# Performance work log

Measured on AMD Instinct MI355X. Metric: run time of the kernel, lower is better.

Reference implementation:

```python
import jax, jax.numpy as jnp
import numpy as np

ITEM_NUM = 50000
EMBED = 256          # d4 = 64, d2 = 128
HIDDEN = 128
BETA = 0.5
BATCH = 4096
HIST = 50
K_NEAR = 10


def setup_inputs() -> dict:
    key = jax.random.key(0)
    ks = jax.random.split(key, 12)
    d4, d2 = EMBED // 4, EMBED // 2
    return {
        "history": jax.random.randint(ks[0], (BATCH, HIST), 0, ITEM_NUM),
        "target": jax.random.randint(ks[1], (BATCH,), 0, ITEM_NUM),
        "near_pois": jax.random.randint(ks[2], (ITEM_NUM, K_NEAR), 0, ITEM_NUM),
        "target_region": jax.random.randint(ks[3], (BATCH,), 0, 1000),
        "E_in": jax.random.normal(ks[4], (ITEM_NUM, d4), jnp.float32) * 0.01,
        "E_out": jax.random.normal(ks[5], (ITEM_NUM, d4), jnp.float32) * 0.01,
        "E_hist": jax.random.normal(ks[6], (ITEM_NUM, d2), jnp.float32) * 0.01,
        "E_targ": jax.random.normal(ks[7], (ITEM_NUM, d2), jnp.float32) * 0.01,
        "W1": jax.random.normal(ks[8], (HIDDEN, EMBED), jnp.float32) * 0.02,
        "b1": jnp.zeros((HIDDEN,), jnp.float32),
        "W2": jax.random.normal(ks[9], (1, HIDDEN), jnp.float32) * 0.02,
    }


def _self_attn(q_src, kv):
    # q = row 0 of q_src; key is a RESHAPE (not transpose) of kv, faithful to torch code.
    N, K, d = kv.shape
    q = q_src[:, 0:1, :]                      # [N,1,d]
    k = kv.reshape(N, d, K)                   # [N,d,K] (reshape, matching torch)
    scores = jnp.einsum('nod,ndk->nok', q, k) / jnp.sqrt(jnp.float32(d))
    w = jax.nn.softmax(scores, axis=-1)       # [N,1,K]
    return jnp.einsum('nok,nkd->nod', w, kv)[:, 0, :]  # [N,d]


def reference(history, target, near_pois, target_region,
              E_in, E_out, E_hist, E_targ, W1, b1, W2):
    ingoing = E_in[near_pois]                 # [N,K,d4]
    outgoing = E_out[near_pois]               # [N,K,d4]
    region_out = _self_attn(ingoing, outgoing)   # [N,d4]
    region_in = _self_attn(outgoing, ingoing)    # [N,d4]

    hist_region = jnp.concatenate([region_in[history], region_out[history]], -1)  # [B,H,d2]
    targ_region = jnp.concatenate([region_out[target], region_in[target]], -1)    # [B,d2]

    hist = jnp.concatenate([E_hist[history], hist_region], -1)      # [B,H,E]
    targ = jnp.concatenate([E_targ[target], targ_region], -1)       # [B,E]

    x = hist * targ[:, None, :]                                     # [B,H,E]
    h1 = jax.nn.relu(x @ W1.T + b1)                                 # [B,H,hidden] (dropout = eval/identity)
    scores = (h1 @ W2.T)[..., 0]                                    # [B,H]

    mask = (history != target[:, None])
    expA = jnp.exp(scores) * mask                                   # [B,H]
    denom = jnp.sum(expA, axis=-1) ** BETA                          # [B], power-normalized (non-softmax)
    w = expA / denom[:, None]                                       # [B,H]

    pred = jnp.einsum('bhe,bh,be->b', hist, w, targ)                # weighted bmm reduction
    return jax.nn.sigmoid(pred)
```

## Files before the change

### kernel.cpp

```cpp
#include <hip/hip_runtime.h>
#include <hip/hip_bf16.h>
#include <math.h>

#define EMBED 256
#define HIDDEN 128
#define NBATCH 4096
#define HISTN 50
#define KNEAR 10
#define D4 64
#define ITEMN 50000
#define XSB 272
#define RBLK (ITEMN / 4)

#define SH 64.0f
#define SW 32.0f
#define INV_SXSW (1.0f / 32768.0f)
#define INV_SX (1.0f / 1024.0f)

typedef __attribute__((ext_vector_type(4))) float floatx4;
typedef __attribute__((ext_vector_type(2))) float floatx2;
typedef __attribute__((ext_vector_type(2))) __fp16 half2v;

__device__ inline unsigned pkh2(float a, float b) {
    union { half2v h; unsigned u; } cv;
    cv.h = __builtin_amdgcn_cvt_pkrtz(a, b);
    return cv.u;
}
__device__ inline float h2f(unsigned short u) {
    union { unsigned short u; __fp16 h; } cv; cv.u = u;
    return (float)cv.h;
}
__device__ inline unsigned pk_fp8x4(float a, float b, float c, float d) {
    int v = __builtin_amdgcn_cvt_pk_fp8_f32(a, b, 0, false);
    v = __builtin_amdgcn_cvt_pk_fp8_f32(c, d, v, true);
    return (unsigned)v;
}
__device__ inline void up_fp8x4(unsigned u, float* f) {
    floatx2 lo = __builtin_amdgcn_cvt_pk_f32_fp8((int)u, false);
    floatx2 hi = __builtin_amdgcn_cvt_pk_f32_fp8((int)u, true);
    f[0] = lo.x; f[1] = lo.y; f[2] = hi.x; f[3] = hi.y;
}

template<int CTRL>
__device__ __forceinline__ float dppf(float x) {
    return __uint_as_float((unsigned)__builtin_amdgcn_update_dpp(
        0, (int)__float_as_uint(x), CTRL, 0xF, 0xF, true));
}
#define DPP_XOR1 0xB1
#define DPP_XOR2 0x4E
#define DPP_HMIR 0x141
#define DPP_MIR  0x140

__global__ __launch_bounds__(256) void prep_eio(
    const float* __restrict__ E_in, const float* __restrict__ E_out,
    unsigned short* __restrict__ EioT)
{
    int tid = blockIdx.x * 256 + threadIdx.x;
    int row = tid >> 4, c = tid & 15;
    const float* src = (c < 8) ? &E_in[(size_t)row * 64 + (c & 7) * 8]
                               : &E_out[(size_t)row * 64 + (c & 7) * 8];
    float4 a = ((const float4*)src)[0];
    float4 b = ((const float4*)src)[1];
    uint4 o;
    o.x = pkh2(a.x, a.y); o.y = pkh2(a.z, a.w);
    o.z = pkh2(b.x, b.y); o.w = pkh2(b.z, b.w);
    *(uint4*)&EioT[(size_t)row * 128 + c * 8] = o;
}

__global__ __launch_bounds__(256) void regions3(
    const int* __restrict__ np,
    const unsigned short* __restrict__ EioT,
    const float* __restrict__ E_hist, const float* __restrict__ W1,
    unsigned char* __restrict__ histT, unsigned char* __restrict__ W1s)
{
    __shared__ unsigned short tiles[4][2][KNEAR * D4];

    if (blockIdx.x < RBLK) {
        const int wv = threadIdx.x >> 6;
        const int lane = threadIdx.x & 63;
        const int n = blockIdx.x * 4 + wv;
        const int g16 = lane >> 4, c16 = lane & 15;
        const int half = c16 >> 3, col = (c16 & 7) * 8;

#pragma unroll
        for (int j = 0; j < 3; ++j) {
            int r = j * 4 + g16;
            if (r < KNEAR) {
                int item = np[n * KNEAR + r];
                uint4 v = *(const uint4*)&EioT[(size_t)item * 128 + c16 * 8];
                *(uint4*)&tiles[wv][half][r * 64 + col] = v;
            }
        }
        __asm__ volatile("s_waitcnt lgkmcnt(0)" ::: "memory");

        const int kk = c16;
        const int par = lane & 1, cp = lane >> 1;

#pragma unroll
        for (int pass = 0; pass < 2; ++pass) {
            const unsigned short* qrow = tiles[wv][pass];
            const unsigned short* kvt = tiles[wv][1 - pass];

            float qf[16];
            {
                uint4 qa = *(const uint4*)&qrow[g16 * 16];
                uint4 qb = *(const uint4*)&qrow[g16 * 16 + 8];
                unsigned wd[8] = {qa.x, qa.y, qa.z, qa.w, qb.x, qb.y, qb.z, qb.w};
#pragma unroll
                for (int m = 0; m < 8; ++m) {
                    qf[2 * m]     = h2f((unsigned short)(wd[m] & 0xffff));
                    qf[2 * m + 1] = h2f((unsigned short)(wd[m] >> 16));
                }
            }

            const unsigned short* kvp = &kvt[g16 * 160 + kk];
            float p = 0.f;
#pragma unroll
            for (int i = 0; i < 16; ++i)
                p = fmaf(h2f(kvp[10 * i]), qf[i], p);
            p += __shfl_xor(p, 16);
            p += __shfl_xor(p, 32);
            float sc = p * 0.125f;

            float mv = (kk < 10) ? sc : -1e30f;
            mv = fmaxf(mv, dppf<DPP_XOR1>(mv));
            mv = fmaxf(mv, dppf<DPP_XOR2>(mv));
            mv = fmaxf(mv, dppf<DPP_HMIR>(mv));
            mv = fmaxf(mv, dppf<DPP_MIR>(mv));
            float e = (kk < 10) ? __expf(sc - mv) : 0.f;
            float s = e;
            s += dppf<DPP_XOR1>(s);
            s += dppf<DPP_XOR2>(s);
            s += dppf<DPP_HMIR>(s);
            s += dppf<DPP_MIR>(s);
            float w = e / s;

            float oc0 = 0.f, oc1 = 0.f;
#pragma unroll
            for (int q = 0; q < 5; ++q) {
                float we = __uint_as_float(__builtin_amdgcn_readlane(__float_as_uint(w), 2 * q));
                float wo = __uint_as_float(__builtin_amdgcn_readlane(__float_as_uint(w), 2 * q + 1));
                float ws = par ? wo : we;
                unsigned v = *(const unsigned*)&kvt[(2 * q + par) * 64 + cp * 2];
                oc0 = fmaf(h2f((unsigned short)(v & 0xffff)), ws, oc0);
                oc1 = fmaf(h2f((unsigned short)(v >> 16)), ws, oc1);
            }
            oc0 += dppf<DPP_XOR1>(oc0);
            oc1 += dppf<DPP_XOR1>(oc1);
            if (!par) {
                unsigned char* dst = histT + (size_t)n * 256
                                     + (pass ? 128 : 192) + cp * 2;
                int v2 = __builtin_amdgcn_cvt_pk_fp8_f32(oc0 * SH, oc1 * SH, 0, false);
                *(unsigned short*)dst = (unsigned short)(v2 & 0xffff);
            }
        }
        return;
    }

    long t = (long)(blockIdx.x - RBLK) * 256 + threadIdx.x;
    if (t < (long)ITEMN * 16) {
        int row = (int)(t >> 4);
        int c8 = ((int)t & 15) * 8;
        const float4* s = (const float4*)&E_hist[(size_t)row * 128 + c8];
        float4 a = s[0], b = s[1];
        uint2 o;
        o.x = pk_fp8x4(a.x * SH, a.y * SH, a.z * SH, a.w * SH);
        o.y = pk_fp8x4(b.x * SH, b.y * SH, b.z * SH, b.w * SH);
        *(uint2*)&histT[(size_t)row * 256 + c8] = o;
        return;
    }
    t -= (long)ITEMN * 16;
    if (t < 4096) {
        int l = (int)t & 63;
        int f = (int)t >> 6;
        int k = f >> 3, nt = f & 7;
        int row = nt * 16 + (l & 15);
        int col = k * 32 + ((l >> 4) << 3);
        const float* src = W1 + row * EMBED + col;
        uint2 o;
        o.x = pk_fp8x4(src[0] * SW, src[1] * SW, src[2] * SW, src[3] * SW);
        o.y = pk_fp8x4(src[4] * SW, src[5] * SW, src[6] * SW, src[7] * SW);
        *(uint2*)&W1s[(size_t)t * 8] = o;
    }
}

__global__ __launch_bounds__(256, 6) void score_kernel(
    const int* __restrict__ history, const int* __restrict__ target,
    const unsigned char* __restrict__ histT,
    const float* __restrict__ E_targ,
    const unsigned char* __restrict__ W1s,
    const float* __restrict__ b1, const float* __restrict__ W2,
    float* __restrict__ out)
{
    __shared__ __align__(16) unsigned char Xs[64][XSB];
    __shared__ float scoreP[4][64];
    __shared__ float rowsumS[64];

    const int t = threadIdx.x;
    const int lane = t & 63;
    const int wv = t >> 6;
    const int b = blockIdx.x;
    const int ti = target[b];
    const int nt0 = wv * 2;
    const int c4 = lane * 4;

    unsigned uu[13];
    int hrow[13];
#pragma unroll
    for (int j = 0; j < 13; ++j) {
        int h = wv + j * 4;
        hrow[j] = h;
        if (h < HISTN) {
            int item = history[b * HISTN + h];
            uu[j] = *(const unsigned*)&histT[(size_t)item * 256 + c4];
        }
    }

    float tgs[4];
    if (c4 < 128) {
        float4 v = *(const float4*)&E_targ[(size_t)ti * 128 + c4];
        tgs[0] = v.x * 16.f; tgs[1] = v.y * 16.f;
        tgs[2] = v.z * 16.f; tgs[3] = v.w * 16.f;
    } else {
        int src = (c4 < 192) ? (c4 + 64) : (c4 - 64);
        unsigned u = *(const unsigned*)&histT[(size_t)ti * 256 + src];
        float f[4]; up_fp8x4(u, f);
        tgs[0] = f[0] * 0.25f; tgs[1] = f[1] * 0.25f;
        tgs[2] = f[2] * 0.25f; tgs[3] = f[3] * 0.25f;
    }

#pragma unroll
    for (int j = 0; j < 13; ++j) {
        if (hrow[j] < HISTN) {
            float f[4]; up_fp8x4(uu[j], f);
            *(unsigned*)&Xs[hrow[j]][c4] =
                pk_fp8x4(f[0] * tgs[0], f[1] * tgs[1], f[2] * tgs[2], f[3] * tgs[3]);
        }
    }
    __syncthreads();

    floatx4 acc[4][2];
    floatx4 accr = (floatx4){0.f, 0.f, 0.f, 0.f};
#pragma unroll
    for (int m = 0; m < 4; ++m)
#pragma unroll
        for (int n = 0; n < 2; ++n) acc[m][n] = (floatx4){0.f, 0.f, 0.f, 0.f};

    const int ar = lane & 15;
    const int kb8 = (lane >> 4) << 3;
    const long* W1f = (const long*)W1s;
    const long ones = 0x3838383838383838L;

#pragma unroll
    for (int k = 0; k < 8; ++k) {
        long a0 = *(const long*)&Xs[ar][k * 32 + kb8];
        long a1 = *(const long*)&Xs[16 + ar][k * 32 + kb8];
        long a2 = *(const long*)&Xs[32 + ar][k * 32 + kb8];
        long a3 = *(const long*)&Xs[48 + ar][k * 32 + kb8];
        long ax = *(const long*)&Xs[wv * 16 + ar][k * 32 + kb8];
        long bq0 = W1f[(k * 8 + nt0) * 64 + lane];
        long bq1 = W1f[(k * 8 + nt0 + 1) * 64 + lane];
        acc[0][0] = __builtin_amdgcn_mfma_f32_16x16x32_fp8_fp8(a0, bq0, acc[0][0], 0, 0, 0);
        acc[0][1] = __builtin_amdgcn_mfma_f32_16x16x32_fp8_fp8(a0, bq1, acc[0][1], 0, 0, 0);
        acc[1][0] = __builtin_amdgcn_mfma_f32_16x16x32_fp8_fp8(a1, bq0, acc[1][0], 0, 0, 0);
        acc[1][1] = __builtin_amdgcn_mfma_f32_16x16x32_fp8_fp8(a1, bq1, acc[1][1], 0, 0, 0);
        acc[2][0] = __builtin_amdgcn_mfma_f32_16x16x32_fp8_fp8(a2, bq0, acc[2][0], 0, 0, 0);
        acc[2][1] = __builtin_amdgcn_mfma_f32_16x16x32_fp8_fp8(a2, bq1, acc[2][1], 0, 0, 0);
        acc[3][0] = __builtin_amdgcn_mfma_f32_16x16x32_fp8_fp8(a3, bq0, acc[3][0], 0, 0, 0);
        acc[3][1] = __builtin_amdgcn_mfma_f32_16x16x32_fp8_fp8(a3, bq1, acc[3][1], 0, 0, 0);
        accr      = __builtin_amdgcn_mfma_f32_16x16x32_fp8_fp8(ax, ones, accr, 0, 0, 0);
    }

    if (ar == 0) {
        int hb = wv * 16 + ((lane >> 4) << 2);
        rowsumS[hb + 0] = accr[0] * INV_SX;
        rowsumS[hb + 1] = accr[1] * INV_SX;
        rowsumS[hb + 2] = accr[2] * INV_SX;
        rowsumS[hb + 3] = accr[3] * INV_SX;
    }

    float w2v[2], b1v[2];
#pragma unroll
    for (int n = 0; n < 2; ++n) {
        int o = (nt0 + n) * 16 + ar;
        w2v[n] = W2[o];
        b1v[n] = b1[o];
    }
#pragma unroll
    for (int m = 0; m < 4; ++m) {
        float p[4] = {0.f, 0.f, 0.f, 0.f};
#pragma unroll
        for (int n = 0; n < 2; ++n)
#pragma unroll
            for (int r = 0; r < 4; ++r)
                p[r] += w2v[n] * fmaxf(acc[m][n][r] * INV_SXSW + b1v[n], 0.f);
#pragma unroll
        for (int r = 0; r < 4; ++r) {
            float v = p[r];
            v += __shfl_xor(v, 1); v += __shfl_xor(v, 2);
            v += __shfl_xor(v, 4); v += __shfl_xor(v, 8);
            if (ar == 0) scoreP[wv][m * 16 + ((lane >> 4) << 2) + r] = v;
        }
    }
    __syncthreads();

    if (wv == 0) {
        float e = 0.f, er = 0.f;
        if (lane < HISTN) {
            int item = history[b * HISTN + lane];
            float sc = scoreP[0][lane] + scoreP[1][lane] + scoreP[2][lane] + scoreP[3][lane];
            e = (item != ti) ? expf(sc) : 0.f;
            er = e * rowsumS[lane];
        }
#pragma unroll
        for (int off = 1; off < 64; off <<= 1) {
            e += __shfl_xor(e, off);
            er += __shfl_xor(er, off);
        }
        if (lane == 0) {
            float pred = er / sqrtf(e);
            out[b] = 1.f / (1.f + expf(-pred));
        }
    }
}

extern "C" void kernel_launch(void* const* d_in, const int* in_sizes, int n_in,
                              void* d_out, int out_size, void* d_ws, size_t ws_size,
                              hipStream_t stream) {
    const int* history = (const int*)d_in[0];
    const int* target = (const int*)d_in[1];
    const int* near_pois = (const int*)d_in[2];
    const float* E_in = (const float*)d_in[4];
    const float* E_out = (const float*)d_in[5];
    const float* E_hist = (const float*)d_in[6];
    const float* E_targ = (const float*)d_in[7];
    const float* W1 = (const float*)d_in[8];
    const float* b1 = (const float*)d_in[9];
    const float* W2 = (const float*)d_in[10];
    float* out = (float*)d_out;

    unsigned char* W1s = (unsigned char*)d_ws;
    unsigned char* histT = W1s + 32768;
    unsigned short* EioT = (unsigned short*)(histT + (size_t)ITEMN * 256);

    prep_eio<<<(ITEMN * 16) / 256, 256, 0, stream>>>(E_in, E_out, EioT);

    const int tailBlocks = (int)(((long)ITEMN * 16 + 4096 + 255) / 256);
    regions3<<<RBLK + tailBlocks, 256, 0, stream>>>(
        near_pois, EioT, E_hist, W1, histT, W1s);

    score_kernel<<<NBATCH, 256, 0, stream>>>(
        history, target, histT, E_targ, W1s, b1, W2, out);
}
```

Before: 69.18 us.

## Remap region attention to per-lane dot contributions with wave-wide DPP reductions

Each lane now loads one query element and the five contiguous kv dwords that the reshape maps to it, forms ten partial products, and reduces each across the wave with DPP row/broadcast steps. All lanes read the ten scores via readlane and compute the softmax redundantly in registers, folding the normalisation into the final fp8 scale. This replaces strided LDS reads, cross-lane shuffles and per-weight readlanes, at the cost of ten full-wave DPP reduction chains per pass.

```diff
diff --git a/kernel.cpp b/kernel.cpp
--- a/kernel.cpp
+++ b/kernel.cpp
@@ -50,6 +50,8 @@
 #define DPP_XOR2 0x4E
 #define DPP_HMIR 0x141
 #define DPP_MIR  0x140
+#define DPP_BC15 0x142
+#define DPP_BC31 0x143
 
 __global__ __launch_bounds__(256) void prep_eio(
     const float* __restrict__ E_in, const float* __restrict__ E_out,
@@ -67,20 +69,20 @@
     *(uint4*)&EioT[(size_t)row * 128 + c * 8] = o;
 }
 
-__global__ __launch_bounds__(256) void regions3(
+__global__ __launch_bounds__(256) void regions5(
     const int* __restrict__ np,
     const unsigned short* __restrict__ EioT,
     const float* __restrict__ E_hist, const float* __restrict__ W1,
     unsigned char* __restrict__ histT, unsigned char* __restrict__ W1s)
 {
-    __shared__ unsigned short tiles[4][2][KNEAR * D4];
+    __shared__ __align__(16) unsigned short tiles[4][2][KNEAR * D4];
 
     if (blockIdx.x < RBLK) {
         const int wv = threadIdx.x >> 6;
         const int lane = threadIdx.x & 63;
         const int n = blockIdx.x * 4 + wv;
         const int g16 = lane >> 4, c16 = lane & 15;
-        const int half = c16 >> 3, col = (c16 & 7) * 8;
+        const int half = c16 >> 3, colw = c16 & 7;
 
 #pragma unroll
         for (int j = 0; j < 3; ++j) {
@@ -88,12 +90,11 @@
             if (r < KNEAR) {
                 int item = np[n * KNEAR + r];
                 uint4 v = *(const uint4*)&EioT[(size_t)item * 128 + c16 * 8];
-                *(uint4*)&tiles[wv][half][r * 64 + col] = v;
+                *(uint4*)&tiles[wv][half][r * 64 + colw * 8] = v;
             }
         }
         __asm__ volatile("s_waitcnt lgkmcnt(0)" ::: "memory");
 
-        const int kk = c16;
         const int par = lane & 1, cp = lane >> 1;
 
 #pragma unroll
@@ -101,56 +102,65 @@
             const unsigned short* qrow = tiles[wv][pass];
             const unsigned short* kvt = tiles[wv][1 - pass];
 
-            float qf[16];
-            {
-                uint4 qa = *(const uint4*)&qrow[g16 * 16];
-                uint4 qb = *(const uint4*)&qrow[g16 * 16 + 8];
-                unsigned wd[8] = {qa.x, qa.y, qa.z, qa.w, qb.x, qb.y, qb.z, qb.w};
-#pragma unroll
-                for (int m = 0; m < 8; ++m) {
-                    qf[2 * m]     = h2f((unsigned short)(wd[m] & 0xffff));
-                    qf[2 * m + 1] = h2f((unsigned short)(wd[m] >> 16));
-                }
+            float qf = h2f(qrow[lane]);
+            const unsigned* kv32 = (const unsigned*)kvt;
+            unsigned e0 = kv32[5 * lane + 0];
+            unsigned e1 = kv32[5 * lane + 1];
+            unsigned e2 = kv32[5 * lane + 2];
+            unsigned e3 = kv32[5 * lane + 3];
+            unsigned e4 = kv32[5 * lane + 4];
+            float p[10];
+            p[0] = qf * h2f((unsigned short)(e0 & 0xffff));
+            p[1] = qf * h2f((unsigned short)(e0 >> 16));
+            p[2] = qf * h2f((unsigned short)(e1 & 0xffff));
+            p[3] = qf * h2f((unsigned short)(e1 >> 16));
+            p[4] = qf * h2f((unsigned short)(e2 & 0xffff));
+            p[5] = qf * h2f((unsigned short)(e2 >> 16));
+            p[6] = qf * h2f((unsigned short)(e3 & 0xffff));
+            p[7] = qf * h2f((unsigned short)(e3 >> 16));
+            p[8] = qf * h2f((unsigned short)(e4 & 0xffff));
+            p[9] = qf * h2f((unsigned short)(e4 >> 16));
+
+#pragma unroll
+            for (int kk = 0; kk < 10; ++kk) {
+                float v = p[kk];
+                v += dppf<DPP_XOR1>(v);
+                v += dppf<DPP_XOR2>(v);
+                v += dppf<DPP_HMIR>(v);
+                v += dppf<DPP_MIR>(v);
+                v += dppf<DPP_BC15>(v);
+                v += dppf<DPP_BC31>(v);
+                p[kk] = v;
             }
 
-            const unsigned short* kvp = &kvt[g16 * 160 + kk];
-            float p = 0.f;
-#pragma unroll
-            for (int i = 0; i < 16; ++i)
-                p = fmaf(h2f(kvp[10 * i]), qf[i], p);
-            p += __shfl_xor(p, 16);
-            p += __shfl_xor(p, 32);
-            float sc = p * 0.125f;
-
-            float mv = (kk < 10) ? sc : -1e30f;
-            mv = fmaxf(mv, dppf<DPP_XOR1>(mv));
-            mv = fmaxf(mv, dppf<DPP_XOR2>(mv));
-            mv = fmaxf(mv, dppf<DPP_HMIR>(mv));
-            mv = fmaxf(mv, dppf<DPP_MIR>(mv));
-            float e = (kk < 10) ? __expf(sc - mv) : 0.f;
-            float s = e;
-            s += dppf<DPP_XOR1>(s);
-            s += dppf<DPP_XOR2>(s);
-            s += dppf<DPP_HMIR>(s);
-            s += dppf<DPP_MIR>(s);
-            float w = e / s;
+            float sc[10];
+#pragma unroll
+            for (int kk = 0; kk < 10; ++kk)
+                sc[kk] = __uint_as_float(__builtin_amdgcn_readlane(
+                             __float_as_uint(p[kk]), 63)) * 0.125f;
+            float mv = sc[0];
+#pragma unroll
+            for (int kk = 1; kk < 10; ++kk) mv = fmaxf(mv, sc[kk]);
+            float w[10];
+            float s = 0.f;
+#pragma unroll
+            for (int kk = 0; kk < 10; ++kk) { w[kk] = __expf(sc[kk] - mv); s += w[kk]; }
 
             float oc0 = 0.f, oc1 = 0.f;
 #pragma unroll
-            for (int q = 0; q < 5; ++q) {
-                float we = __uint_as_float(__builtin_amdgcn_readlane(__float_as_uint(w), 2 * q));
-                float wo = __uint_as_float(__builtin_amdgcn_readlane(__float_as_uint(w), 2 * q + 1));
-                float ws = par ? wo : we;
-                unsigned v = *(const unsigned*)&kvt[(2 * q + par) * 64 + cp * 2];
+            for (int q2 = 0; q2 < 5; ++q2) {
+                float ws = par ? w[2 * q2 + 1] : w[2 * q2];
+                unsigned v = *(const unsigned*)&kvt[(2 * q2 + par) * 64 + cp * 2];
                 oc0 = fmaf(h2f((unsigned short)(v & 0xffff)), ws, oc0);
                 oc1 = fmaf(h2f((unsigned short)(v >> 16)), ws, oc1);
             }
             oc0 += dppf<DPP_XOR1>(oc0);
             oc1 += dppf<DPP_XOR1>(oc1);
             if (!par) {
+                float scl = SH / s;
                 unsigned char* dst = histT + (size_t)n * 256
                                      + (pass ? 128 : 192) + cp * 2;
-                int v2 = __builtin_amdgcn_cvt_pk_fp8_f32(oc0 * SH, oc1 * SH, 0, false);
+                int v2 = __builtin_amdgcn_cvt_pk_fp8_f32(oc0 * scl, oc1 * scl, 0, false);
                 *(unsigned short*)dst = (unsigned short)(v2 & 0xffff);
             }
         }
@@ -346,7 +356,7 @@
     prep_eio<<<(ITEMN * 16) / 256, 256, 0, stream>>>(E_in, E_out, EioT);
 
     const int tailBlocks = (int)(((long)ITEMN * 16 + 4096 + 255) / 256);
-    regions3<<<RBLK + tailBlocks, 256, 0, stream>>>(
+    regions5<<<RBLK + tailBlocks, 256, 0, stream>>>(
         near_pois, EioT, E_hist, W1, histT, W1s);
 
     score_kernel<<<NBATCH, 256, 0, stream>>>(
```

Measured after the change: 96.36 us. 39.3% more time.
